# Optimization experiments

Hardware: AMD Instinct MI355X
Metric: run time of the kernel (lower is better)

Reference implementation:

```python
import jax, jax.numpy as jnp
import numpy as np

B, DIM, H, W = 16, 512, 32, 32
C = 256          # internal channels = int(512*0.5)
HEADS = 4        # max(1, 256//64)
KD = 32          # key_dim = int(64*0.5)
HD = 64          # head_dim = 256//4
SCALE = KD ** -0.5


def _silu(x):
    return x * jax.nn.sigmoid(x)


def conv1x1(x, Wm, s, b, act):
    # 1x1 conv + folded eval-mode BN (scale/shift) + optional SiLU
    y = jnp.einsum('bchw,oc->bohw', x, Wm)
    y = y * s[None, :, None, None] + b[None, :, None, None]
    return _silu(y) if act else y


def dwconv3(x, Wd, s, b):
    # depthwise 3x3 conv (groups = channels) + BN scale/shift, no act
    y = jax.lax.conv_general_dilated(
        x, Wd, window_strides=(1, 1), padding='SAME',
        feature_group_count=x.shape[1],
        dimension_numbers=('NCHW', 'OIHW', 'NCHW'))
    return y * s[None, :, None, None] + b[None, :, None, None]


def _mk_conv(key, c_out, c_in, k=1):
    k1, k2, k3 = jax.random.split(key, 3)
    fan_in = c_in * k * k
    if k == 1:
        Wm = jax.random.normal(k1, (c_out, c_in), jnp.float32) * fan_in ** -0.5
    else:
        Wm = jax.random.normal(k1, (c_out, c_in, k, k), jnp.float32) * fan_in ** -0.5
    s = jax.random.uniform(k2, (c_out,), jnp.float32, 0.5, 1.5)
    b = 0.1 * jax.random.normal(k3, (c_out,), jnp.float32)
    return Wm, s, b


def setup_inputs() -> dict:
    key = jax.random.key(0)
    ks = jax.random.split(key, 8)
    x = jax.random.normal(ks[0], (B, DIM, H, W), jnp.float32)
    W_cv1, s_cv1, b_cv1 = _mk_conv(ks[1], 2 * C, DIM)
    W_qkv, s_qkv, b_qkv = _mk_conv(ks[2], C + 2 * HEADS * KD, C)  # 512 out
    W_proj, s_proj, b_proj = _mk_conv(ks[3], C, C)
    # depthwise 3x3: OIHW with I=1, groups=C
    W_pe, s_pe, b_pe = _mk_conv(ks[4], C, 1, k=3)
    W_ffn1, s_ffn1, b_ffn1 = _mk_conv(ks[5], 2 * C, C)
    W_ffn2, s_ffn2, b_ffn2 = _mk_conv(ks[6], C, 2 * C)
    W_cv2, s_cv2, b_cv2 = _mk_conv(ks[7], DIM, 2 * C)
    return {
        'x': x,
        'W_cv1': W_cv1, 's_cv1': s_cv1, 'b_cv1': b_cv1,
        'W_qkv': W_qkv, 's_qkv': s_qkv, 'b_qkv': b_qkv,
        'W_proj': W_proj, 's_proj': s_proj, 'b_proj': b_proj,
        'W_pe': W_pe, 's_pe': s_pe, 'b_pe': b_pe,
        'W_ffn1': W_ffn1, 's_ffn1': s_ffn1, 'b_ffn1': b_ffn1,
        'W_ffn2': W_ffn2, 's_ffn2': s_ffn2, 'b_ffn2': b_ffn2,
        'W_cv2': W_cv2, 's_cv2': s_cv2, 'b_cv2': b_cv2,
    }


def reference(x,
              W_cv1, s_cv1, b_cv1,
              W_qkv, s_qkv, b_qkv,
              W_proj, s_proj, b_proj,
              W_pe, s_pe, b_pe,
              W_ffn1, s_ffn1, b_ffn1,
              W_ffn2, s_ffn2, b_ffn2,
              W_cv2, s_cv2, b_cv2):
    bsz, _, h, w = x.shape
    n = h * w
    y = conv1x1(x, W_cv1, s_cv1, b_cv1, act=True)          # [b, 2C, h, w]
    a, bb = y[:, :C], y[:, C:]

    # ----- Attention on bb -----
    qkv = conv1x1(bb, W_qkv, s_qkv, b_qkv, act=False)       # [b, 2*h*kd + C, h, w]
    qkv = qkv.reshape(bsz, HEADS, 2 * KD + HD, n)
    q, k, v = qkv[:, :, :KD], qkv[:, :, KD:2 * KD], qkv[:, :, 2 * KD:]
    attn = jnp.einsum('bhdn,bhdm->bhnm', q, k) * SCALE      # [b, heads, n, n]
    attn = jax.nn.softmax(attn, axis=-1)
    xa = jnp.einsum('bhdm,bhnm->bhdn', v, attn).reshape(bsz, C, h, w)
    xa = xa + dwconv3(v.reshape(bsz, C, h, w), W_pe, s_pe, b_pe)
    xa = conv1x1(xa, W_proj, s_proj, b_proj, act=False)
    bb = bb + xa

    # ----- FFN on bb -----
    ff = conv1x1(bb, W_ffn1, s_ffn1, b_ffn1, act=True)
    ff = conv1x1(ff, W_ffn2, s_ffn2, b_ffn2, act=False)
    bb = bb + ff

    return conv1x1(jnp.concatenate([a, bb], axis=1), W_cv2, s_cv2, b_cv2, act=True)
```

## Files before the change

kernel.cpp:

```cpp
#include <hip/hip_runtime.h>

typedef unsigned short u16;
typedef __attribute__((ext_vector_type(8))) short short8;
typedef __attribute__((ext_vector_type(4))) float f32x4;
typedef __attribute__((ext_vector_type(4))) unsigned int uint4v;
typedef __attribute__((ext_vector_type(4))) unsigned short ushort4v;

#define N_PIX 1024
constexpr float SCALE = 0.17677669529663687f;

__device__ __forceinline__ float bf2f(u16 v) {
    unsigned u = ((unsigned)v) << 16;
    return __builtin_bit_cast(float, u);
}
__device__ __forceinline__ u16 f2bf(float f) {
    unsigned u = __builtin_bit_cast(unsigned, f);
    u += 0x7fff + ((u >> 16) & 1);
    return (u16)(u >> 16);
}
__device__ __forceinline__ float silu_f(float x) { return x / (1.f + __expf(-x)); }

__device__ __forceinline__ f32x4 mfma16(short8 a, short8 b, f32x4 c) {
    return __builtin_amdgcn_mfma_f32_16x16x32_bf16(a, b, c, 0, 0, 0);
}

__device__ __forceinline__ void gl_lds16(const u16* g, u16* l) {
    __builtin_amdgcn_global_load_lds(
        (const __attribute__((address_space(1))) unsigned int*)g,
        (__attribute__((address_space(3))) unsigned int*)l, 16, 0, 0);
}

__global__ void cvtw_k(const float* s0, u16* d0, int n0,
                       const float* s1, u16* d1, int n1,
                       const float* s2, u16* d2, int n2,
                       const float* s3, u16* d3, int n3,
                       const float* s4, u16* d4, int n4,
                       const float* s5, u16* d5, int n5)
{
    const float* sp = nullptr; u16* dp = nullptr; int n = 0;
    switch (blockIdx.y) {
        case 0: sp = s0; dp = d0; n = n0; break;
        case 1: sp = s1; dp = d1; n = n1; break;
        case 2: sp = s2; dp = d2; n = n2; break;
        case 3: sp = s3; dp = d3; n = n3; break;
        case 4: sp = s4; dp = d4; n = n4; break;
        case 5: sp = s5; dp = d5; n = n5; break;
    }
    for (int i = blockIdx.x * 256 + threadIdx.x; i < n; i += gridDim.x * 256)
        dp[i] = f2bf(sp[i]);
}

__global__ __launch_bounds__(256) void trans_k(const float* __restrict__ x, u16* __restrict__ xt)
{
    __shared__ float LT[64 * 65];
    const int tid = threadIdx.x;
    const int n0 = blockIdx.x * 64;
    const int c0 = blockIdx.y * 64;
    const int b  = blockIdx.z;
    const int w = tid >> 6, ln = tid & 63;
#pragma unroll
    for (int s = 0; s < 16; ++s) {
        int c = s * 4 + w;
        LT[c * 65 + ln] = x[((size_t)(b * 512 + c0 + c)) * N_PIX + n0 + ln];
    }
    __syncthreads();
#pragma unroll
    for (int s = 0; s < 16; ++s) {
        int n = s * 4 + w;
        xt[((size_t)(b * N_PIX + n0 + n)) * 512 + c0 + ln] = f2bf(LT[ln * 65 + n]);
    }
}

__global__ __launch_bounds__(512) void gemm_k(
    const u16* __restrict__ Xt, int xcs, int xcoff,
    const u16* __restrict__ Wb, int Cin,
    const float* __restrict__ sc, const float* __restrict__ bi,
    const u16* __restrict__ res, int rcs, int rcoff,
    u16* __restrict__ out, int ocs, int ocoff,
    float* __restrict__ out32,
    u16* __restrict__ vsep,
    int act)
{
    __shared__ __align__(16) u16 WT[2][128 * 32];
    __shared__ __align__(16) u16 XT[2][128 * 32];
    const int tid  = threadIdx.x;
    const int lane = tid & 63;
    const int w    = __builtin_amdgcn_readfirstlane(tid >> 6);
    const int wr = w & 3;
    const int wc = w >> 2;
    const int n0 = blockIdx.x * 128;
    const int o0 = blockIdx.y * 128;
    const int b  = blockIdx.z;
    const int l4 = lane >> 4, l15 = lane & 15;

    const int srow = tid >> 2;
    const int skc  = (tid & 3) * 8;
    const u16* wg = Wb + (size_t)(o0 + srow) * Cin + skc;
    const u16* xg = Xt + ((size_t)(b * N_PIX + n0 + srow)) * xcs + xcoff + skc;

    f32x4 acc[2][4];
#pragma unroll
    for (int i = 0; i < 2; ++i)
#pragma unroll
        for (int j = 0; j < 4; ++j) acc[i][j] = (f32x4){0.f, 0.f, 0.f, 0.f};

    const int nk = Cin >> 5;
    gl_lds16(wg, &WT[0][tid * 8]);
    gl_lds16(xg, &XT[0][tid * 8]);
    __syncthreads();

    for (int kk = 0; kk < nk; ++kk) {
        const int cur = kk & 1;
        if (kk + 1 < nk) {
            const int cc = (kk + 1) << 5;
            gl_lds16(wg + cc, &WT[cur ^ 1][tid * 8]);
            gl_lds16(xg + cc, &XT[cur ^ 1][tid * 8]);
        }
        short8 af[2], bfr[4];
#pragma unroll
        for (int i = 0; i < 2; ++i)
            af[i] = *(const short8*)&WT[cur][(wr * 32 + i * 16 + l15) * 32 + l4 * 8];
#pragma unroll
        for (int j = 0; j < 4; ++j)
            bfr[j] = *(const short8*)&XT[cur][(wc * 64 + j * 16 + l15) * 32 + l4 * 8];
#pragma unroll
        for (int i = 0; i < 2; ++i)
#pragma unroll
            for (int j = 0; j < 4; ++j)
                acc[i][j] = mfma16(af[i], bfr[j], acc[i][j]);
        __syncthreads();
    }

    if (out32) {
        const int Cout = gridDim.y * 128;
        float* eplds = (float*)XT;
        const int row = tid >> 4, cb = (tid & 15) * 8;
#pragma unroll
        for (int h = 0; h < 4; ++h) {
            if (wr == h) {
#pragma unroll
                for (int i = 0; i < 2; ++i)
#pragma unroll
                    for (int j = 0; j < 4; ++j)
#pragma unroll
                        for (int r = 0; r < 4; ++r) {
                            const int oo = i * 16 + l4 * 4 + r;
                            const int go = o0 + h * 32 + oo;
                            float v = acc[i][j][r] * sc[go] + bi[go];
                            if (act) v = silu_f(v);
                            eplds[oo * 128 + wc * 64 + j * 16 + l15] = v;
                        }
            }
            __syncthreads();
            const size_t gidx = ((size_t)b * Cout + o0 + h * 32 + row) * N_PIX + n0 + cb;
            f32x4 a0 = *(const f32x4*)&eplds[row * 128 + cb];
            f32x4 a1 = *(const f32x4*)&eplds[row * 128 + cb + 4];
            *(f32x4*)&out32[gidx]     = a0;
            *(f32x4*)&out32[gidx + 4] = a1;
            __syncthreads();
        }
        return;
    }

    const bool is_v = (vsep != nullptr) && (wr >= 2);
#pragma unroll
    for (int i = 0; i < 2; ++i) {
        const int ob = o0 + wr * 32 + i * 16 + l4 * 4;
        float s4[4], b4[4];
#pragma unroll
        for (int r = 0; r < 4; ++r) { s4[r] = sc[ob + r]; b4[r] = bi[ob + r]; }
#pragma unroll
        for (int j = 0; j < 4; ++j) {
            const int n = n0 + wc * 64 + j * 16 + l15;
            float v[4];
#pragma unroll
            for (int r = 0; r < 4; ++r) {
                v[r] = acc[i][j][r] * s4[r] + b4[r];
                if (act) v[r] = silu_f(v[r]);
            }
            if (is_v) {
                const int hh = ob >> 7;
                const int dv = (ob & 127) - 64;
                u16* vp = vsep + (((size_t)(b * 4 + hh)) * 64 + dv) * N_PIX + n;
#pragma unroll
                for (int r = 0; r < 4; ++r) vp[r * N_PIX] = f2bf(v[r]);
            } else {
                const size_t base = ((size_t)(b * N_PIX + n)) * ocs + ocoff + ob;
                if (res) {
                    ushort4v rr = *(const ushort4v*)&res[((size_t)(b * N_PIX + n)) * rcs + rcoff + ob];
#pragma unroll
                    for (int r = 0; r < 4; ++r) v[r] += bf2f(rr[r]);
                }
                ushort4v pk;
#pragma unroll
                for (int r = 0; r < 4; ++r) pk[r] = f2bf(v[r]);
                *(ushort4v*)&out[base] = pk;
            }
        }
    }
}

__global__ __launch_bounds__(256) void attn_k(
    const u16* __restrict__ qkvt, const u16* __restrict__ vsep,
    u16* __restrict__ xat)
{
    __shared__ __align__(16) u16 KT[2][64 * 40];
    __shared__ __align__(16) u16 VT[2][64 * 72];
    __shared__ __align__(16) u16 PL[4 * 16 * 72];
    const int tid  = threadIdx.x;
    const int lane = tid & 63;
    const int w    = __builtin_amdgcn_readfirstlane(tid >> 6);
    const int l4 = lane >> 4, l15 = lane & 15;
    const int h = blockIdx.y, b = blockIdx.z;
    const int n0w = blockIdx.x * 64 + w * 16;
    u16* PLw = PL + w * 16 * 72;

    const short8 qf = *(const short8*)&qkvt[((size_t)(b * N_PIX + n0w + l15)) * 512 + h * 128 + l4 * 8];

    const int skr = tid >> 2, skc = (tid & 3) * 8;
    const int svd = tid >> 3, svm = (tid & 7) * 8;
    const u16* kgbase = qkvt + ((size_t)(b * N_PIX + skr)) * 512 + h * 128 + 32 + skc;
    const u16* vgbase = vsep + (((size_t)(b * 4 + h)) * 64 + svd) * N_PIX + svm;

    float mrun[4], lrun[4];
#pragma unroll
    for (int r = 0; r < 4; ++r) { mrun[r] = -1e30f; lrun[r] = 0.f; }
    f32x4 accv[4];
#pragma unroll
    for (int d = 0; d < 4; ++d) accv[d] = (f32x4){0.f, 0.f, 0.f, 0.f};
    const f32x4 z4 = {0.f, 0.f, 0.f, 0.f};

    uint4v kreg = *(const uint4v*)(kgbase);
    uint4v vr0  = *(const uint4v*)(vgbase);
    uint4v vr1  = *(const uint4v*)(vgbase + 32 * N_PIX);

    for (int t = 0; t < 16; ++t) {
        const int cur = t & 1;
        *(uint4v*)&KT[cur][skr * 40 + skc] = kreg;
        *(uint4v*)&VT[cur][svd * 72 + svm] = vr0;
        *(uint4v*)&VT[cur][(svd + 32) * 72 + svm] = vr1;
        if (t < 15) {
            const int m1 = (t + 1) * 64;
            kreg = *(const uint4v*)(kgbase + (size_t)m1 * 512);
            vr0  = *(const uint4v*)(vgbase + m1);
            vr1  = *(const uint4v*)(vgbase + 32 * N_PIX + m1);
        }
        __syncthreads();

        f32x4 s[4];
        __builtin_amdgcn_s_setprio(1);
#pragma unroll
        for (int mt = 0; mt < 4; ++mt) {
            short8 kf = *(const short8*)&KT[cur][(mt * 16 + l15) * 40 + l4 * 8];
            s[mt] = mfma16(qf, kf, z4);
        }
        __builtin_amdgcn_s_setprio(0);

        float tm[4];
#pragma unroll
        for (int r = 0; r < 4; ++r) {
            float m_ = fmaxf(fmaxf(s[0][r], s[1][r]), fmaxf(s[2][r], s[3][r]));
            m_ = fmaxf(m_, __shfl_xor(m_, 1));
            m_ = fmaxf(m_, __shfl_xor(m_, 2));
            m_ = fmaxf(m_, __shfl_xor(m_, 4));
            m_ = fmaxf(m_, __shfl_xor(m_, 8));
            tm[r] = m_ * SCALE;
        }
#pragma unroll
        for (int r = 0; r < 4; ++r) {
            float mnew = fmaxf(mrun[r], tm[r]);
            float corr = __expf(mrun[r] - mnew);
            mrun[r] = mnew;
            lrun[r] *= corr;
#pragma unroll
            for (int d = 0; d < 4; ++d) accv[d][r] *= corr;
        }
#pragma unroll
        for (int mt = 0; mt < 4; ++mt)
#pragma unroll
            for (int r = 0; r < 4; ++r) {
                float p = __expf(s[mt][r] * SCALE - mrun[r]);
                lrun[r] += p;
                PLw[(l4 * 4 + r) * 72 + mt * 16 + l15] = f2bf(p);
            }

        __builtin_amdgcn_s_setprio(1);
#pragma unroll
        for (int mq = 0; mq < 2; ++mq) {
            short8 pa = *(const short8*)&PLw[l15 * 72 + mq * 32 + l4 * 8];
#pragma unroll
            for (int d = 0; d < 4; ++d) {
                short8 vf = *(const short8*)&VT[cur][(d * 16 + l15) * 72 + mq * 32 + l4 * 8];
                accv[d] = mfma16(pa, vf, accv[d]);
            }
        }
        __builtin_amdgcn_s_setprio(0);
    }

#pragma unroll
    for (int r = 0; r < 4; ++r) {
        float sum = lrun[r];
        sum += __shfl_xor(sum, 1);
        sum += __shfl_xor(sum, 2);
        sum += __shfl_xor(sum, 4);
        sum += __shfl_xor(sum, 8);
        lrun[r] = 1.f / sum;
    }
#pragma unroll
    for (int d = 0; d < 4; ++d)
#pragma unroll
        for (int r = 0; r < 4; ++r) {
            const int n = n0w + l4 * 4 + r;
            xat[((size_t)(b * N_PIX + n)) * 256 + h * 64 + d * 16 + l15] =
                f2bf(accv[d][r] * lrun[r]);
        }
}

__global__ __launch_bounds__(256) void pe_k(
    const u16* __restrict__ vsep, const float* __restrict__ Wpe,
    const float* __restrict__ spe, const float* __restrict__ bpe,
    u16* __restrict__ xat)
{
    const int t  = threadIdx.x;
    const int y0 = blockIdx.x * 2;
    const int b  = blockIdx.y;
    const u16* vp = vsep + ((size_t)(b * 256 + t)) * N_PIX;

    float rv[128];
#pragma unroll
    for (int rr = 0; rr < 4; ++rr) {
        const int yy = y0 - 1 + rr;
        if (yy >= 0 && yy < 32) {
#pragma unroll
            for (int g = 0; g < 4; ++g) {
                uint4v u = *(const uint4v*)&vp[yy * 32 + g * 8];
#pragma unroll
                for (int e = 0; e < 4; ++e) {
                    rv[rr * 32 + g * 8 + e * 2]     = bf2f((u16)(u[e] & 0xffff));
                    rv[rr * 32 + g * 8 + e * 2 + 1] = bf2f((u16)(u[e] >> 16));
                }
            }
        } else {
#pragma unroll
            for (int j = 0; j < 32; ++j) rv[rr * 32 + j] = 0.f;
        }
    }
    float w9[9];
#pragma unroll
    for (int i = 0; i < 9; ++i) w9[i] = Wpe[t * 9 + i];
    const float scv = spe[t], biv = bpe[t];
    u16* xp = xat + ((size_t)(b * N_PIX)) * 256 + t;

#pragma unroll
    for (int py = 0; py < 2; ++py)
#pragma unroll
        for (int px = 0; px < 32; ++px) {
            float a = 0.f;
#pragma unroll
            for (int ky = 0; ky < 3; ++ky) {
                const int lr = py + ky;
#pragma unroll
                for (int kx = 0; kx < 3; ++kx) {
                    const int xx = px + kx - 1;
                    if (xx >= 0 && xx < 32)
                        a = fmaf(w9[ky * 3 + kx], rv[lr * 32 + xx], a);
                }
            }
            const int n = (y0 + py) * 32 + px;
            u16* p = xp + (size_t)n * 256;
            *p = f2bf(bf2f(*p) + a * scv + biv);
        }
}

extern "C" void kernel_launch(void* const* d_in, const int* in_sizes, int n_in,
                              void* d_out, int out_size, void* d_ws, size_t ws_size,
                              hipStream_t stream)
{
    const float* x      = (const float*)d_in[0];
    const float* W_cv1  = (const float*)d_in[1];
    const float* s_cv1  = (const float*)d_in[2];
    const float* b_cv1  = (const float*)d_in[3];
    const float* W_qkv  = (const float*)d_in[4];
    const float* s_qkv  = (const float*)d_in[5];
    const float* b_qkv  = (const float*)d_in[6];
    const float* W_proj = (const float*)d_in[7];
    const float* s_proj = (const float*)d_in[8];
    const float* b_proj = (const float*)d_in[9];
    const float* W_pe   = (const float*)d_in[10];
    const float* s_pe   = (const float*)d_in[11];
    const float* b_pe   = (const float*)d_in[12];
    const float* W_ffn1 = (const float*)d_in[13];
    const float* s_ffn1 = (const float*)d_in[14];
    const float* b_ffn1 = (const float*)d_in[15];
    const float* W_ffn2 = (const float*)d_in[16];
    const float* s_ffn2 = (const float*)d_in[17];
    const float* b_ffn2 = (const float*)d_in[18];
    const float* W_cv2  = (const float*)d_in[19];
    const float* s_cv2  = (const float*)d_in[20];
    const float* b_cv2  = (const float*)d_in[21];

    u16* ws = (u16*)d_ws;
    u16* xt      = ws;
    u16* yt      = xt + 8388608;
    u16* qkvt    = yt + 8388608;
    u16* fft     = qkvt + 8388608;
    u16* vsep    = fft + 8388608;
    u16* xat     = vsep + 4194304;
    u16* wb_cv1  = xat + 4194304;
    u16* wb_qkv  = wb_cv1 + 262144;
    u16* wb_proj = wb_qkv + 131072;
    u16* wb_ffn1 = wb_proj + 65536;
    u16* wb_ffn2 = wb_ffn1 + 131072;
    u16* wb_cv2  = wb_ffn2 + 131072;

    cvtw_k<<<dim3(64, 6), 256, 0, stream>>>(
        W_cv1, wb_cv1, 512 * 512, W_qkv, wb_qkv, 512 * 256,
        W_proj, wb_proj, 256 * 256, W_ffn1, wb_ffn1, 512 * 256,
        W_ffn2, wb_ffn2, 256 * 512, W_cv2, wb_cv2, 512 * 512);
    trans_k<<<dim3(16, 8, 16), 256, 0, stream>>>(x, xt);

    gemm_k<<<dim3(8, 4, 16), 512, 0, stream>>>(
        xt, 512, 0, wb_cv1, 512, s_cv1, b_cv1,
        nullptr, 0, 0, yt, 512, 0, nullptr, nullptr, 1);
    gemm_k<<<dim3(8, 4, 16), 512, 0, stream>>>(
        yt, 512, 256, wb_qkv, 256, s_qkv, b_qkv,
        nullptr, 0, 0, qkvt, 512, 0, nullptr, vsep, 0);
    attn_k<<<dim3(16, 4, 16), 256, 0, stream>>>(qkvt, vsep, xat);
    pe_k<<<dim3(16, 16), 256, 0, stream>>>(vsep, W_pe, s_pe, b_pe, xat);
    gemm_k<<<dim3(8, 2, 16), 512, 0, stream>>>(
        xat, 256, 0, wb_proj, 256, s_proj, b_proj,
        yt, 512, 256, yt, 512, 256, nullptr, nullptr, 0);
    gemm_k<<<dim3(8, 4, 16), 512, 0, stream>>>(
        yt, 512, 256, wb_ffn1, 256, s_ffn1, b_ffn1,
        nullptr, 0, 0, fft, 512, 0, nullptr, nullptr, 1);
    gemm_k<<<dim3(8, 2, 16), 512, 0, stream>>>(
        fft, 512, 0, wb_ffn2, 512, s_ffn2, b_ffn2,
        yt, 512, 256, yt, 512, 256, nullptr, nullptr, 0);
    gemm_k<<<dim3(8, 4, 16), 512, 0, stream>>>(
        yt, 512, 0, wb_cv2, 512, s_cv2, b_cv2,
        nullptr, 0, 0, nullptr, 0, 0, (float*)d_out, nullptr, 1);
}
```

Before: 279.1 us.

## Load attention K/V fragments directly from global, fold scale into Q, lazy rescale

The attention kernel drops its LDS staging and barriers for K and V and has each wave load its MFMA fragments straight from global memory. The softmax scale and log2(e) are folded into the Q projection epilogue so exp2 can be used directly. Cross-lane max/sum reductions switch from shuffles to DPP moves, and the running-max rescale is skipped when the new max exceeds the old by no more than a threshold. This removes LDS traffic and syncs but duplicates global K/V reads across the four waves and relies on L2 caching; the lazy rescale risks overflow only for large score jumps.

```diff
diff --git a/kernel.cpp b/kernel.cpp
--- a/kernel.cpp
+++ b/kernel.cpp
@@ -8,6 +8,7 @@
 
 #define N_PIX 1024
 constexpr float SCALE = 0.17677669529663687f;
+constexpr float QSC   = 0.25506626725324577f;
 
 __device__ __forceinline__ float bf2f(u16 v) {
     unsigned u = ((unsigned)v) << 16;
@@ -20,6 +21,10 @@
 }
 __device__ __forceinline__ float silu_f(float x) { return x / (1.f + __expf(-x)); }
 
+__device__ __forceinline__ float exp2_f(float x) {
+    float r; asm("v_exp_f32 %0, %1" : "=v"(r) : "v"(x)); return r;
+}
+
 __device__ __forceinline__ f32x4 mfma16(short8 a, short8 b, f32x4 c) {
     return __builtin_amdgcn_mfma_f32_16x16x32_bf16(a, b, c, 0, 0, 0);
 }
@@ -28,6 +33,29 @@
     __builtin_amdgcn_global_load_lds(
         (const __attribute__((address_space(1))) unsigned int*)g,
         (__attribute__((address_space(3))) unsigned int*)l, 16, 0, 0);
+}
+
+__device__ __forceinline__ float dpp_max16(float x) {
+    int v = __builtin_bit_cast(int, x);
+    x = fmaxf(x, __builtin_bit_cast(float, __builtin_amdgcn_mov_dpp(v, 0xB1, 0xF, 0xF, true)));
+    v = __builtin_bit_cast(int, x);
+    x = fmaxf(x, __builtin_bit_cast(float, __builtin_amdgcn_mov_dpp(v, 0x4E, 0xF, 0xF, true)));
+    v = __builtin_bit_cast(int, x);
+    x = fmaxf(x, __builtin_bit_cast(float, __builtin_amdgcn_mov_dpp(v, 0x141, 0xF, 0xF, true)));
+    v = __builtin_bit_cast(int, x);
+    x = fmaxf(x, __builtin_bit_cast(float, __builtin_amdgcn_mov_dpp(v, 0x140, 0xF, 0xF, true)));
+    return x;
+}
+__device__ __forceinline__ float dpp_sum16(float x) {
+    int v = __builtin_bit_cast(int, x);
+    x += __builtin_bit_cast(float, __builtin_amdgcn_mov_dpp(v, 0xB1, 0xF, 0xF, true));
+    v = __builtin_bit_cast(int, x);
+    x += __builtin_bit_cast(float, __builtin_amdgcn_mov_dpp(v, 0x4E, 0xF, 0xF, true));
+    v = __builtin_bit_cast(int, x);
+    x += __builtin_bit_cast(float, __builtin_amdgcn_mov_dpp(v, 0x141, 0xF, 0xF, true));
+    v = __builtin_bit_cast(int, x);
+    x += __builtin_bit_cast(float, __builtin_amdgcn_mov_dpp(v, 0x140, 0xF, 0xF, true));
+    return x;
 }
 
 __global__ void cvtw_k(const float* s0, u16* d0, int n0,
@@ -136,8 +164,8 @@
         float* eplds = (float*)XT;
         const int row = tid >> 4, cb = (tid & 15) * 8;
 #pragma unroll
-        for (int h = 0; h < 4; ++h) {
-            if (wr == h) {
+        for (int hh = 0; hh < 4; ++hh) {
+            if (wr == hh) {
 #pragma unroll
                 for (int i = 0; i < 2; ++i)
 #pragma unroll
@@ -145,14 +173,14 @@
 #pragma unroll
                         for (int r = 0; r < 4; ++r) {
                             const int oo = i * 16 + l4 * 4 + r;
-                            const int go = o0 + h * 32 + oo;
+                            const int go = o0 + hh * 32 + oo;
                             float v = acc[i][j][r] * sc[go] + bi[go];
                             if (act) v = silu_f(v);
                             eplds[oo * 128 + wc * 64 + j * 16 + l15] = v;
                         }
             }
             __syncthreads();
-            const size_t gidx = ((size_t)b * Cout + o0 + h * 32 + row) * N_PIX + n0 + cb;
+            const size_t gidx = ((size_t)b * Cout + o0 + hh * 32 + row) * N_PIX + n0 + cb;
             f32x4 a0 = *(const f32x4*)&eplds[row * 128 + cb];
             f32x4 a1 = *(const f32x4*)&eplds[row * 128 + cb + 4];
             *(f32x4*)&out32[gidx]     = a0;
@@ -163,12 +191,13 @@
     }
 
     const bool is_v = (vsep != nullptr) && (wr >= 2);
+    const float qmul = (vsep != nullptr && wr == 0) ? QSC : 1.f;
 #pragma unroll
     for (int i = 0; i < 2; ++i) {
         const int ob = o0 + wr * 32 + i * 16 + l4 * 4;
         float s4[4], b4[4];
 #pragma unroll
-        for (int r = 0; r < 4; ++r) { s4[r] = sc[ob + r]; b4[r] = bi[ob + r]; }
+        for (int r = 0; r < 4; ++r) { s4[r] = sc[ob + r] * qmul; b4[r] = bi[ob + r] * qmul; }
 #pragma unroll
         for (int j = 0; j < 4; ++j) {
             const int n = n0 + wc * 64 + j * 16 + l15;
@@ -200,12 +229,10 @@
     }
 }
 
-__global__ __launch_bounds__(256) void attn_k(
+__global__ __launch_bounds__(256, 4) void attn_k(
     const u16* __restrict__ qkvt, const u16* __restrict__ vsep,
     u16* __restrict__ xat)
 {
-    __shared__ __align__(16) u16 KT[2][64 * 40];
-    __shared__ __align__(16) u16 VT[2][64 * 72];
     __shared__ __align__(16) u16 PL[4 * 16 * 72];
     const int tid  = threadIdx.x;
     const int lane = tid & 63;
@@ -216,11 +243,8 @@
     u16* PLw = PL + w * 16 * 72;
 
     const short8 qf = *(const short8*)&qkvt[((size_t)(b * N_PIX + n0w + l15)) * 512 + h * 128 + l4 * 8];
-
-    const int skr = tid >> 2, skc = (tid & 3) * 8;
-    const int svd = tid >> 3, svm = (tid & 7) * 8;
-    const u16* kgbase = qkvt + ((size_t)(b * N_PIX + skr)) * 512 + h * 128 + 32 + skc;
-    const u16* vgbase = vsep + (((size_t)(b * 4 + h)) * 64 + svd) * N_PIX + svm;
+    const u16* kb = qkvt + ((size_t)(b * N_PIX + l15)) * 512 + h * 128 + 32 + l4 * 8;
+    const u16* vb = vsep + (((size_t)(b * 4 + h)) * 64 + l15) * N_PIX + l4 * 8;
 
     float mrun[4], lrun[4];
 #pragma unroll
@@ -230,56 +254,48 @@
     for (int d = 0; d < 4; ++d) accv[d] = (f32x4){0.f, 0.f, 0.f, 0.f};
     const f32x4 z4 = {0.f, 0.f, 0.f, 0.f};
 
-    uint4v kreg = *(const uint4v*)(kgbase);
-    uint4v vr0  = *(const uint4v*)(vgbase);
-    uint4v vr1  = *(const uint4v*)(vgbase + 32 * N_PIX);
-
     for (int t = 0; t < 16; ++t) {
-        const int cur = t & 1;
-        *(uint4v*)&KT[cur][skr * 40 + skc] = kreg;
-        *(uint4v*)&VT[cur][svd * 72 + svm] = vr0;
-        *(uint4v*)&VT[cur][(svd + 32) * 72 + svm] = vr1;
-        if (t < 15) {
-            const int m1 = (t + 1) * 64;
-            kreg = *(const uint4v*)(kgbase + (size_t)m1 * 512);
-            vr0  = *(const uint4v*)(vgbase + m1);
-            vr1  = *(const uint4v*)(vgbase + 32 * N_PIX + m1);
-        }
-        __syncthreads();
+        const int m0 = t * 64;
+        short8 kf[4];
+#pragma unroll
+        for (int mt = 0; mt < 4; ++mt)
+            kf[mt] = *(const short8*)(kb + (size_t)(m0 + mt * 16) * 512);
+        short8 vf[2][4];
+#pragma unroll
+        for (int mq = 0; mq < 2; ++mq)
+#pragma unroll
+            for (int d = 0; d < 4; ++d)
+                vf[mq][d] = *(const short8*)(vb + (size_t)(d * 16) * N_PIX + m0 + mq * 32);
 
         f32x4 s[4];
         __builtin_amdgcn_s_setprio(1);
 #pragma unroll
-        for (int mt = 0; mt < 4; ++mt) {
-            short8 kf = *(const short8*)&KT[cur][(mt * 16 + l15) * 40 + l4 * 8];
-            s[mt] = mfma16(qf, kf, z4);
-        }
+        for (int mt = 0; mt < 4; ++mt) s[mt] = mfma16(qf, kf[mt], z4);
         __builtin_amdgcn_s_setprio(0);
 
-        float tm[4];
+        float tm[4], g = -1e30f;
 #pragma unroll
         for (int r = 0; r < 4; ++r) {
             float m_ = fmaxf(fmaxf(s[0][r], s[1][r]), fmaxf(s[2][r], s[3][r]));
-            m_ = fmaxf(m_, __shfl_xor(m_, 1));
-            m_ = fmaxf(m_, __shfl_xor(m_, 2));
-            m_ = fmaxf(m_, __shfl_xor(m_, 4));
-            m_ = fmaxf(m_, __shfl_xor(m_, 8));
-            tm[r] = m_ * SCALE;
-        }
-#pragma unroll
-        for (int r = 0; r < 4; ++r) {
-            float mnew = fmaxf(mrun[r], tm[r]);
-            float corr = __expf(mrun[r] - mnew);
-            mrun[r] = mnew;
-            lrun[r] *= corr;
-#pragma unroll
-            for (int d = 0; d < 4; ++d) accv[d][r] *= corr;
+            tm[r] = dpp_max16(m_);
+            g = fmaxf(g, tm[r] - mrun[r]);
+        }
+        if (!__all(g <= 11.0f)) {
+#pragma unroll
+            for (int r = 0; r < 4; ++r) {
+                float mnew = fmaxf(mrun[r], tm[r]);
+                float corr = exp2_f(mrun[r] - mnew);
+                mrun[r] = mnew;
+                lrun[r] *= corr;
+#pragma unroll
+                for (int d = 0; d < 4; ++d) accv[d][r] *= corr;
+            }
         }
 #pragma unroll
         for (int mt = 0; mt < 4; ++mt)
 #pragma unroll
             for (int r = 0; r < 4; ++r) {
-                float p = __expf(s[mt][r] * SCALE - mrun[r]);
+                float p = exp2_f(s[mt][r] - mrun[r]);
                 lrun[r] += p;
                 PLw[(l4 * 4 + r) * 72 + mt * 16 + l15] = f2bf(p);
             }
@@ -289,23 +305,15 @@
         for (int mq = 0; mq < 2; ++mq) {
             short8 pa = *(const short8*)&PLw[l15 * 72 + mq * 32 + l4 * 8];
 #pragma unroll
-            for (int d = 0; d < 4; ++d) {
-                short8 vf = *(const short8*)&VT[cur][(d * 16 + l15) * 72 + mq * 32 + l4 * 8];
-                accv[d] = mfma16(pa, vf, accv[d]);
-            }
+            for (int d = 0; d < 4; ++d)
+                accv[d] = mfma16(pa, vf[mq][d], accv[d]);
         }
         __builtin_amdgcn_s_setprio(0);
     }
 
 #pragma unroll
-    for (int r = 0; r < 4; ++r) {
-        float sum = lrun[r];
-        sum += __shfl_xor(sum, 1);
-        sum += __shfl_xor(sum, 2);
-        sum += __shfl_xor(sum, 4);
-        sum += __shfl_xor(sum, 8);
-        lrun[r] = 1.f / sum;
-    }
+    for (int r = 0; r < 4; ++r)
+        lrun[r] = 1.f / dpp_sum16(lrun[r]);
 #pragma unroll
     for (int d = 0; d < 4; ++d)
 #pragma unroll
```

Result: slower. 320.3 us (+14.8%).
